# Kernel tuning notes

Measured on AMD Instinct MI355X. Metric: run time of the kernel, lower is better.

The kernel has to match this reference:

```python
import jax, jax.numpy as jnp
import numpy as np

N_NODES = 50000
N_EDGES = 800000
D = 256
N_GRAPHS = 128
N_CLASSES = 2


def gcn_conv(x, W, b, src, dst, ew):
    # PyG GCNConv: add self-loops (weight 1), symmetric norm D^-1/2 (A+I) D^-1/2, then X@W + b
    n = x.shape[0]
    deg = jax.ops.segment_sum(ew, dst, num_segments=n) + 1.0  # includes self-loop weight
    dinv = jnp.where(deg > 0, jax.lax.rsqrt(deg), 0.0)
    xw = x @ W  # [N, D_out]
    norm = dinv[src] * ew * dinv[dst]  # [E]
    msgs = xw[src] * norm[:, None]  # [E, D_out] gathered messages
    agg = jax.ops.segment_sum(msgs, dst, num_segments=n)
    agg = agg + xw * (dinv * dinv)[:, None]  # self-loop contribution
    return agg + b


def setup_inputs() -> dict:
    key = jax.random.key(0)
    ks = jax.random.split(key, 16)
    emb_x = jax.random.normal(ks[0], (N_NODES, D), dtype=jnp.float32)
    edge_index = jax.random.randint(ks[1], (2, N_EDGES), 0, N_NODES, dtype=jnp.int64)
    edge_weight = jax.random.uniform(ks[2], (N_EDGES,), dtype=jnp.float32)
    batch = jnp.sort(jax.random.randint(ks[3], (N_NODES,), 0, N_GRAPHS, dtype=jnp.int64))
    s = 1.0 / np.sqrt(D)
    params = {}
    for i, k in enumerate(ks[4:7]):
        params[f"W{i+1}"] = jax.random.normal(k, (D, D), dtype=jnp.float32) * s
        params[f"b{i+1}"] = jnp.zeros((D,), dtype=jnp.float32)
    params["fc1_w"] = jax.random.normal(ks[7], (2 * D, D), dtype=jnp.float32) / np.sqrt(2 * D)
    params["fc1_b"] = jnp.zeros((D,), dtype=jnp.float32)
    params["fc2_w"] = jax.random.normal(ks[8], (D, N_CLASSES), dtype=jnp.float32) * s
    params["fc2_b"] = jnp.zeros((N_CLASSES,), dtype=jnp.float32)
    return dict(emb_x=emb_x, edge_index=edge_index, edge_weight=edge_weight, batch=batch, **params)


def reference(emb_x, edge_index, edge_weight, batch, W1, b1, W2, b2, W3, b3, fc1_w, fc1_b, fc2_w, fc2_b):
    src, dst = edge_index[0], edge_index[1]
    x = emb_x
    for W, b in ((W1, b1), (W2, b2), (W3, b3)):
        x = gcn_conv(x, W, b, src, dst, edge_weight)
        x = jax.nn.relu(x)  # dropout is identity in eval mode
    counts = jax.ops.segment_sum(jnp.ones((x.shape[0],), x.dtype), batch, num_segments=N_GRAPHS)
    mean_x = jax.ops.segment_sum(x, batch, num_segments=N_GRAPHS) / jnp.maximum(counts, 1.0)[:, None]
    max_x = jax.ops.segment_max(x, batch, num_segments=N_GRAPHS)
    max_x = jnp.where(jnp.isfinite(max_x), max_x, 0.0)  # empty segments -> 0
    h = jnp.concatenate([mean_x, max_x], axis=1)  # [G, 2D]
    h = jax.nn.relu(h @ fc1_w + fc1_b)
    return h @ fc2_w + fc2_b  # [G, n_classes]
```

## Files before the change

kernel.cpp:

```cpp
#include <hip/hip_runtime.h>
#include <math.h>

#define N_NODES 50000
#define N_PAD 50048
#define N_EDGES 800000
#define DIM 256
#define N_GRAPHS 128

using f32x4 = __attribute__((ext_vector_type(4))) float;
using s16x8 = __attribute__((ext_vector_type(8))) short;

__device__ __forceinline__ ushort bf16_hi(float f) {
  unsigned u = __float_as_uint(f);
  return (ushort)((u + 0x7FFFu + ((u >> 16) & 1u)) >> 16);
}
__device__ __forceinline__ float bf16_up(ushort h) {
  return __uint_as_float(((unsigned)h) << 16);
}
__device__ __forceinline__ void bf16_split(float f, ushort& hh, ushort& ll) {
  hh = bf16_hi(f);
  float d = f - bf16_up(hh);
  ll = bf16_hi(d);
}
__device__ __forceinline__ float up_lo(unsigned u) {
  return __uint_as_float(u << 16);
}
__device__ __forceinline__ float up_hi(unsigned u) {
  return __uint_as_float(u & 0xffff0000u);
}

__global__ __launch_bounds__(256) void count_kernel(
    const int* __restrict__ dst, int* __restrict__ counts,
    int* __restrict__ p_local) {
  int e = blockIdx.x * 256 + threadIdx.x;
  if (e < N_EDGES) p_local[e] = atomicAdd(&counts[dst[e]], 1);
}

#define SCAN_CHUNK 1024
#define SCAN_BLOCKS ((N_NODES + SCAN_CHUNK - 1) / SCAN_CHUNK)

__global__ __launch_bounds__(256) void scan_phaseA(
    const int* __restrict__ counts, int* __restrict__ blockSums) {
  __shared__ int sdata[256];
  int b = blockIdx.x, t = threadIdx.x;
  int base = b * SCAN_CHUNK + t * 4;
  int s = 0;
#pragma unroll
  for (int i = 0; i < 4; ++i) {
    int idx = base + i;
    if (idx < N_NODES) s += counts[idx];
  }
  sdata[t] = s;
  __syncthreads();
  for (int off = 128; off > 0; off >>= 1) {
    if (t < off) sdata[t] += sdata[t + off];
    __syncthreads();
  }
  if (t == 0) blockSums[b] = sdata[0];
}

__global__ void scan_phaseB(int* __restrict__ blockSums, int* __restrict__ rs) {
  if (threadIdx.x == 0 && blockIdx.x == 0) {
    int acc = 0;
    for (int i = 0; i < SCAN_BLOCKS; ++i) {
      int v = blockSums[i];
      blockSums[i] = acc;
      acc += v;
    }
    rs[N_NODES] = acc;
  }
}

__global__ __launch_bounds__(256) void scan_phaseC(
    const int* __restrict__ counts, const int* __restrict__ blockSums,
    int* __restrict__ rs) {
  __shared__ int sdata[256];
  int b = blockIdx.x, t = threadIdx.x;
  int base = b * SCAN_CHUNK + t * 4;
  int v[4];
  int s = 0;
#pragma unroll
  for (int i = 0; i < 4; ++i) {
    int idx = base + i;
    v[i] = (idx < N_NODES) ? counts[idx] : 0;
    s += v[i];
  }
  sdata[t] = s;
  __syncthreads();
  for (int off = 1; off < 256; off <<= 1) {
    int x = (t >= off) ? sdata[t - off] : 0;
    __syncthreads();
    sdata[t] += x;
    __syncthreads();
  }
  int excl = (t == 0) ? 0 : sdata[t - 1];
  int o = blockSums[b] + excl;
#pragma unroll
  for (int i = 0; i < 4; ++i) {
    int idx = base + i;
    if (idx < N_NODES) rs[idx] = o;
    o += v[i];
  }
}

__global__ __launch_bounds__(256) void fill_kernel(
    const int* __restrict__ src, const int* __restrict__ dst,
    const float* __restrict__ ew, const int* __restrict__ rs,
    const int* __restrict__ p_local,
    int* __restrict__ csrc, float* __restrict__ cw) {
  int e = blockIdx.x * 256 + threadIdx.x;
  if (e < N_EDGES) {
    int d = dst[e];
    int pos = rs[d] + p_local[e];
    csrc[pos] = src[e];
    cw[pos] = ew[e];
  }
}

__global__ __launch_bounds__(256) void degsum_kernel(
    const int* __restrict__ rs, const float* __restrict__ cw,
    float* __restrict__ dinv) {
  int n = blockIdx.x * 256 + threadIdx.x;
  if (n >= N_NODES) return;
  int b = rs[n], e = rs[n + 1];
  float s = 1.0f;
  for (int i = b; i < e; ++i) s += cw[i];
  dinv[n] = 1.0f / sqrtf(s);
}

__global__ __launch_bounds__(256) void norm_kernel(
    const int* __restrict__ csrc, const float* __restrict__ dinv,
    float* __restrict__ cw) {
  int e = blockIdx.x * 256 + threadIdx.x;
  if (e < N_EDGES) cw[e] = cw[e] * dinv[csrc[e]];
}

__global__ __launch_bounds__(256) void round_x_kernel(
    const float* __restrict__ x, ushort* __restrict__ tab, int n4) {
  int i = blockIdx.x * 256 + threadIdx.x;
  if (i >= n4) return;
  float4 v = ((const float4*)x)[i];
  ushort4 h;
  h.x = bf16_hi(v.x);
  h.y = bf16_hi(v.y);
  h.z = bf16_hi(v.z);
  h.w = bf16_hi(v.w);
  ((ushort4*)tab)[i] = h;
}

__global__ __launch_bounds__(256) void prep_w_kernel(
    const float* __restrict__ W1, const float* __restrict__ W2, const float* __restrict__ W3,
    ushort* __restrict__ wt) {
  int k = blockIdx.x;
  int w = blockIdx.y;
  int n = threadIdx.x;
  const float* W = (w == 0) ? W1 : (w == 1) ? W2 : W3;
  float v = W[k * 256 + n];
  ushort h, l;
  bf16_split(v, h, l);
  ushort* hplane = wt + (size_t)w * 2 * 256 * 256;
  ushort* lplane = hplane + 256 * 256;
  hplane[n * 256 + k] = h;
  lplane[n * 256 + k] = l;
}

#define GBM 64
#define GBK 32

__device__ __forceinline__ void gload16(const void* g, void* l) {
  __builtin_amdgcn_global_load_lds(
      (const __attribute__((address_space(1))) void*)g,
      (__attribute__((address_space(3))) void*)l, 16, 0, 0);
}

__global__ __launch_bounds__(256) void gemm_mfma(
    const ushort* __restrict__ A,
    const ushort* __restrict__ Wh, const ushort* __restrict__ Wl,
    ushort* __restrict__ C, int M) {
  __shared__ ushort Asl[2][GBM * GBK];
  int tid = threadIdx.x;
  int bm = blockIdx.x * GBM;
  int wave = tid >> 6, lane = tid & 63;
  int wc = wave * 64;
  int l15 = lane & 15;
  int lkb = lane >> 4;

  f32x4 acc[4][4];
#pragma unroll
  for (int i = 0; i < 4; ++i)
#pragma unroll
    for (int j = 0; j < 4; ++j) acc[i][j] = (f32x4){0.f, 0.f, 0.f, 0.f};

  int arow = tid & 63, akb = tid >> 6;

#define STAGE_A(buf, ts)                                                       \
  gload16(A + (size_t)(bm + arow) * 256 + (ts) * 32 + akb * 8,                 \
          &Asl[buf][tid * 8])

  STAGE_A(0, 0);
  __syncthreads();
  int cur = 0;
  for (int t = 0; t < 8; ++t) {
    if (t < 7) STAGE_A(cur ^ 1, t + 1);
    s16x8 af[4], bh[4], bl[4];
#pragma unroll
    for (int f = 0; f < 4; ++f) {
      size_t woff = (size_t)(wc + f * 16 + l15) * 256 + t * 32 + lkb * 8;
      bh[f] = *(const s16x8*)(Wh + woff);
      bl[f] = *(const s16x8*)(Wl + woff);
    }
#pragma unroll
    for (int f = 0; f < 4; ++f)
      af[f] = *(const s16x8*)(&Asl[cur][(lkb * 64 + f * 16 + l15) * 8]);
#pragma unroll
    for (int i = 0; i < 4; ++i)
#pragma unroll
      for (int j = 0; j < 4; ++j) {
        acc[i][j] = __builtin_amdgcn_mfma_f32_16x16x32_bf16(af[i], bh[j], acc[i][j], 0, 0, 0);
        acc[i][j] = __builtin_amdgcn_mfma_f32_16x16x32_bf16(af[i], bl[j], acc[i][j], 0, 0, 0);
      }
    __syncthreads();
    cur ^= 1;
  }
#undef STAGE_A

#pragma unroll
  for (int i = 0; i < 4; ++i) {
    int rbase = bm + i * 16 + (lane >> 4) * 4;
#pragma unroll
    for (int j = 0; j < 4; ++j) {
      int col = wc + j * 16 + l15;
#pragma unroll
      for (int r = 0; r < 4; ++r) {
        int row = rbase + r;
        if (row < M) C[(size_t)row * 256 + col] = bf16_hi(acc[i][j][r]);
      }
    }
  }
}

template <int MODE>
__global__ __launch_bounds__(256) void spmm_row(
    const ushort* __restrict__ xw, const int* __restrict__ rs,
    const int* __restrict__ csrc, const float* __restrict__ cw,
    const float* __restrict__ dinv, const float* __restrict__ bias,
    float* __restrict__ xf32, ushort* __restrict__ xout) {
  int wave = threadIdx.x >> 6, lane = threadIdx.x & 63;
  int n = __builtin_amdgcn_readfirstlane(blockIdx.x * 4 + wave);
  const uint2* base = (const uint2*)xw;
  size_t rowoff = (size_t)n * 64 + lane;
  float a0 = 0.f, a1 = 0.f, a2 = 0.f, a3 = 0.f;
  int beg = __builtin_amdgcn_readfirstlane(rs[n]);
  int end = __builtin_amdgcn_readfirstlane(rs[n + 1]);
  int i = beg;
  for (; i + 8 <= end; i += 8) {
    int idx[8];
    float w[8];
    uint2 v[8];
#pragma unroll
    for (int u = 0; u < 8; ++u) { idx[u] = csrc[i + u]; w[u] = cw[i + u]; }
#pragma unroll
    for (int u = 0; u < 8; ++u) v[u] = base[(size_t)idx[u] * 64 + lane];
#pragma unroll
    for (int u = 0; u < 8; ++u) {
      a0 += w[u] * up_lo(v[u].x);
      a1 += w[u] * up_hi(v[u].x);
      a2 += w[u] * up_lo(v[u].y);
      a3 += w[u] * up_hi(v[u].y);
    }
  }
  for (; i < end; ++i) {
    float w0 = cw[i];
    uint2 v0 = base[(size_t)csrc[i] * 64 + lane];
    a0 += w0 * up_lo(v0.x);
    a1 += w0 * up_hi(v0.x);
    a2 += w0 * up_lo(v0.y);
    a3 += w0 * up_hi(v0.y);
  }
  float di = dinv[n];
  float dd = di * di;
  uint2 sv = base[rowoff];
  float4 b = ((const float4*)bias)[lane];
  float r0 = fmaxf(di * a0 + dd * up_lo(sv.x) + b.x, 0.f);
  float r1 = fmaxf(di * a1 + dd * up_hi(sv.x) + b.y, 0.f);
  float r2 = fmaxf(di * a2 + dd * up_lo(sv.y) + b.z, 0.f);
  float r3 = fmaxf(di * a3 + dd * up_hi(sv.y) + b.w, 0.f);
  if (MODE == 1) {
    float4 r;
    r.x = r0; r.y = r1; r.z = r2; r.w = r3;
    ((float4*)xf32)[rowoff] = r;
  } else {
    uint2 hv;
    hv.x = (unsigned)bf16_hi(r0) | ((unsigned)bf16_hi(r1) << 16);
    hv.y = (unsigned)bf16_hi(r2) | ((unsigned)bf16_hi(r3) << 16);
    ((uint2*)xout)[rowoff] = hv;
  }
}

__device__ __forceinline__ int lower_bound_dev(const int* a, int n, int key) {
  int lo = 0, hi = n;
  while (lo < hi) {
    int mid = (lo + hi) >> 1;
    if (a[mid] < key) lo = mid + 1; else hi = mid;
  }
  return lo;
}

__global__ __launch_bounds__(256) void pool_kernel(
    const float* __restrict__ x, const int* __restrict__ batch,
    float* __restrict__ h) {
  int g = blockIdx.x;
  int dchunk = blockIdx.y;
  int t = threadIdx.x;
  int dl = t & 63;
  int nl = t >> 6;
  int d = dchunk * 64 + dl;
  int start = lower_bound_dev(batch, N_NODES, g);
  int end = lower_bound_dev(batch, N_NODES, g + 1);
  float sum = 0.f, mx = 0.f;
  for (int i = start + nl; i < end; i += 4) {
    float v = x[(size_t)i * DIM + d];
    sum += v;
    mx = fmaxf(mx, v);
  }
  __shared__ float ssum[4][64];
  __shared__ float smax[4][64];
  ssum[nl][dl] = sum;
  smax[nl][dl] = mx;
  __syncthreads();
  if (nl == 0) {
    sum = ssum[0][dl] + ssum[1][dl] + ssum[2][dl] + ssum[3][dl];
    mx = fmaxf(fmaxf(smax[0][dl], smax[1][dl]), fmaxf(smax[2][dl], smax[3][dl]));
    float cnt = (float)(end - start);
    h[(size_t)g * (2 * DIM) + d] = sum / fmaxf(cnt, 1.0f);
    h[(size_t)g * (2 * DIM) + DIM + d] = mx;
  }
}

__global__ __launch_bounds__(256) void fc_kernel(
    const float* __restrict__ h, const float* __restrict__ fc1_w,
    const float* __restrict__ fc1_b, const float* __restrict__ fc2_w,
    const float* __restrict__ fc2_b, float* __restrict__ out) {
  int g = blockIdx.x;
  int j = threadIdx.x;
  __shared__ float hs[2 * DIM];
  __shared__ float s0[256], s1[256];
  hs[j] = h[(size_t)g * (2 * DIM) + j];
  hs[j + 256] = h[(size_t)g * (2 * DIM) + 256 + j];
  __syncthreads();
  float acc = fc1_b[j];
  for (int k = 0; k < 2 * DIM; ++k) acc += hs[k] * fc1_w[(size_t)k * DIM + j];
  float r = fmaxf(acc, 0.0f);
  s0[j] = r * fc2_w[j * 2 + 0];
  s1[j] = r * fc2_w[j * 2 + 1];
  __syncthreads();
  for (int off = 128; off > 0; off >>= 1) {
    if (j < off) { s0[j] += s0[j + off]; s1[j] += s1[j + off]; }
    __syncthreads();
  }
  if (j == 0) {
    out[g * 2 + 0] = s0[0] + fc2_b[0];
    out[g * 2 + 1] = s1[0] + fc2_b[1];
  }
}

extern "C" void kernel_launch(void* const* d_in, const int* in_sizes, int n_in,
                              void* d_out, int out_size, void* d_ws, size_t ws_size,
                              hipStream_t stream) {
  const float* emb_x = (const float*)d_in[0];
  const int* eidx = (const int*)d_in[1];
  const int* esrc = eidx;
  const int* edst = eidx + N_EDGES;
  const float* ew = (const float*)d_in[2];
  const int* batch = (const int*)d_in[3];
  const float* W1 = (const float*)d_in[4];
  const float* b1 = (const float*)d_in[5];
  const float* W2 = (const float*)d_in[6];
  const float* b2 = (const float*)d_in[7];
  const float* W3 = (const float*)d_in[8];
  const float* b3 = (const float*)d_in[9];
  const float* fc1_w = (const float*)d_in[10];
  const float* fc1_b = (const float*)d_in[11];
  const float* fc2_w = (const float*)d_in[12];
  const float* fc2_b = (const float*)d_in[13];
  float* out = (float*)d_out;

  char* ws = (char*)d_ws;
  size_t off = 0;
  auto take = [&](size_t bytes) -> char* {
    char* p = ws + off;
    off = (off + bytes + 255) & ~(size_t)255;
    return p;
  };
  ushort* XW = (ushort*)take((size_t)N_PAD * DIM * 2);
  ushort* Xa = (ushort*)take((size_t)N_PAD * DIM * 2);
  float* Xf32 = (float*)take((size_t)N_NODES * DIM * 4);
  ushort* WT = (ushort*)take((size_t)6 * 256 * 256 * 2);
  float* dinv = (float*)take(N_NODES * 4);
  int* counts = (int*)take(N_NODES * 4);
  int* rs = (int*)take((N_NODES + 1) * 4);
  int* p_local = (int*)take(N_EDGES * 4);
  int* blockSums = (int*)take(64 * 4);
  int* csrc = (int*)take(N_EDGES * 4);
  float* cw = (float*)take(N_EDGES * 4);
  float* h = (float*)take((size_t)N_GRAPHS * 2 * DIM * 4);

  hipMemsetAsync(counts, 0, N_NODES * 4, stream);
  hipMemsetAsync(Xa + (size_t)N_NODES * DIM, 0, (size_t)(N_PAD - N_NODES) * DIM * 2, stream);

  int eblocks = (N_EDGES + 255) / 256;
  int nblocks = (N_NODES + 255) / 256;

  count_kernel<<<eblocks, 256, 0, stream>>>(edst, counts, p_local);
  scan_phaseA<<<SCAN_BLOCKS, 256, 0, stream>>>(counts, blockSums);
  scan_phaseB<<<1, 64, 0, stream>>>(blockSums, rs);
  scan_phaseC<<<SCAN_BLOCKS, 256, 0, stream>>>(counts, blockSums, rs);
  fill_kernel<<<eblocks, 256, 0, stream>>>(esrc, edst, ew, rs, p_local, csrc, cw);
  degsum_kernel<<<nblocks, 256, 0, stream>>>(rs, cw, dinv);
  norm_kernel<<<eblocks, 256, 0, stream>>>(csrc, dinv, cw);

  round_x_kernel<<<(N_NODES * DIM / 4 + 255) / 256, 256, 0, stream>>>(
      emb_x, Xa, N_NODES * DIM / 4);
  prep_w_kernel<<<dim3(256, 3), 256, 0, stream>>>(W1, W2, W3, WT);

  ushort* W1h = WT + 0 * 65536; ushort* W1l = WT + 1 * 65536;
  ushort* W2h = WT + 2 * 65536; ushort* W2l = WT + 3 * 65536;
  ushort* W3h = WT + 4 * 65536; ushort* W3l = WT + 5 * 65536;

  dim3 ggrid(N_PAD / GBM);
  int sgrid = N_NODES / 4;

  gemm_mfma<<<ggrid, 256, 0, stream>>>(Xa, W1h, W1l, XW, N_NODES);
  spmm_row<0><<<sgrid, 256, 0, stream>>>(XW, rs, csrc, cw, dinv, b1, nullptr, Xa);
  gemm_mfma<<<ggrid, 256, 0, stream>>>(Xa, W2h, W2l, XW, N_NODES);
  spmm_row<0><<<sgrid, 256, 0, stream>>>(XW, rs, csrc, cw, dinv, b2, nullptr, Xa);
  gemm_mfma<<<ggrid, 256, 0, stream>>>(Xa, W3h, W3l, XW, N_NODES);
  spmm_row<1><<<sgrid, 256, 0, stream>>>(XW, rs, csrc, cw, dinv, b3, Xf32, nullptr);

  pool_kernel<<<dim3(N_GRAPHS, 4), 256, 0, stream>>>(Xf32, batch, h);
  fc_kernel<<<N_GRAPHS, 256, 0, stream>>>(h, fc1_w, fc1_b, fc2_w, fc2_b, out);
}
```

Measured before the change: 460.9 us.

## Prefetch GEMM weight fragments and use 16-byte gathers in SpMM

Result: no change. 452.1 us (-1.9%).

```diff
diff --git a/kernel.cpp b/kernel.cpp
--- a/kernel.cpp
+++ b/kernel.cpp
@@ -21,12 +21,6 @@
   hh = bf16_hi(f);
   float d = f - bf16_up(hh);
   ll = bf16_hi(d);
-}
-__device__ __forceinline__ float up_lo(unsigned u) {
-  return __uint_as_float(u << 16);
-}
-__device__ __forceinline__ float up_hi(unsigned u) {
-  return __uint_as_float(u & 0xffff0000u);
 }
 
 __global__ __launch_bounds__(256) void count_kernel(
@@ -198,29 +192,39 @@
           &Asl[buf][tid * 8])
 
   STAGE_A(0, 0);
-  __syncthreads();
-  int cur = 0;
+  s16x8 bh_c[4], bl_c[4], bh_n[4], bl_n[4];
+#pragma unroll
+  for (int f = 0; f < 4; ++f) {
+    size_t woff = (size_t)(wc + f * 16 + l15) * 256 + lkb * 8;
+    bh_c[f] = *(const s16x8*)(Wh + woff);
+    bl_c[f] = *(const s16x8*)(Wl + woff);
+  }
+  __syncthreads();
+#pragma unroll
   for (int t = 0; t < 8; ++t) {
-    if (t < 7) STAGE_A(cur ^ 1, t + 1);
-    s16x8 af[4], bh[4], bl[4];
-#pragma unroll
-    for (int f = 0; f < 4; ++f) {
-      size_t woff = (size_t)(wc + f * 16 + l15) * 256 + t * 32 + lkb * 8;
-      bh[f] = *(const s16x8*)(Wh + woff);
-      bl[f] = *(const s16x8*)(Wl + woff);
+    if (t < 7) {
+      STAGE_A((t & 1) ^ 1, t + 1);
+#pragma unroll
+      for (int f = 0; f < 4; ++f) {
+        size_t woff = (size_t)(wc + f * 16 + l15) * 256 + (t + 1) * 32 + lkb * 8;
+        bh_n[f] = *(const s16x8*)(Wh + woff);
+        bl_n[f] = *(const s16x8*)(Wl + woff);
+      }
     }
+    s16x8 af[4];
 #pragma unroll
     for (int f = 0; f < 4; ++f)
-      af[f] = *(const s16x8*)(&Asl[cur][(lkb * 64 + f * 16 + l15) * 8]);
+      af[f] = *(const s16x8*)(&Asl[t & 1][(lkb * 64 + f * 16 + l15) * 8]);
 #pragma unroll
     for (int i = 0; i < 4; ++i)
 #pragma unroll
       for (int j = 0; j < 4; ++j) {
-        acc[i][j] = __builtin_amdgcn_mfma_f32_16x16x32_bf16(af[i], bh[j], acc[i][j], 0, 0, 0);
-        acc[i][j] = __builtin_amdgcn_mfma_f32_16x16x32_bf16(af[i], bl[j], acc[i][j], 0, 0, 0);
+        acc[i][j] = __builtin_amdgcn_mfma_f32_16x16x32_bf16(af[i], bh_c[j], acc[i][j], 0, 0, 0);
+        acc[i][j] = __builtin_amdgcn_mfma_f32_16x16x32_bf16(af[i], bl_c[j], acc[i][j], 0, 0, 0);
       }
     __syncthreads();
-    cur ^= 1;
+#pragma unroll
+    for (int f = 0; f < 4; ++f) { bh_c[f] = bh_n[f]; bl_c[f] = bl_n[f]; }
   }
 #undef STAGE_A
 
@@ -240,60 +244,77 @@
 }
 
 template <int MODE>
-__global__ __launch_bounds__(256) void spmm_row(
+__global__ __launch_bounds__(256) void spmm_row16(
     const ushort* __restrict__ xw, const int* __restrict__ rs,
     const int* __restrict__ csrc, const float* __restrict__ cw,
     const float* __restrict__ dinv, const float* __restrict__ bias,
     float* __restrict__ xf32, ushort* __restrict__ xout) {
   int wave = threadIdx.x >> 6, lane = threadIdx.x & 63;
   int n = __builtin_amdgcn_readfirstlane(blockIdx.x * 4 + wave);
-  const uint2* base = (const uint2*)xw;
-  size_t rowoff = (size_t)n * 64 + lane;
-  float a0 = 0.f, a1 = 0.f, a2 = 0.f, a3 = 0.f;
+  int e2 = lane >> 5;
+  int c = lane & 31;
+  const ushort* chunk = xw + c * 8;
+  float acc[8] = {};
   int beg = __builtin_amdgcn_readfirstlane(rs[n]);
   int end = __builtin_amdgcn_readfirstlane(rs[n + 1]);
   int i = beg;
   for (; i + 8 <= end; i += 8) {
-    int idx[8];
-    float w[8];
-    uint2 v[8];
-#pragma unroll
-    for (int u = 0; u < 8; ++u) { idx[u] = csrc[i + u]; w[u] = cw[i + u]; }
-#pragma unroll
-    for (int u = 0; u < 8; ++u) v[u] = base[(size_t)idx[u] * 64 + lane];
-#pragma unroll
-    for (int u = 0; u < 8; ++u) {
-      a0 += w[u] * up_lo(v[u].x);
-      a1 += w[u] * up_hi(v[u].x);
-      a2 += w[u] * up_lo(v[u].y);
-      a3 += w[u] * up_hi(v[u].y);
+    int idx[4];
+    float w[4];
+    s16x8 v[4];
+#pragma unroll
+    for (int u = 0; u < 4; ++u) {
+      idx[u] = csrc[i + 2 * u + e2];
+      w[u] = cw[i + 2 * u + e2];
     }
-  }
-  for (; i < end; ++i) {
-    float w0 = cw[i];
-    uint2 v0 = base[(size_t)csrc[i] * 64 + lane];
-    a0 += w0 * up_lo(v0.x);
-    a1 += w0 * up_hi(v0.x);
-    a2 += w0 * up_lo(v0.y);
-    a3 += w0 * up_hi(v0.y);
-  }
-  float di = dinv[n];
-  float dd = di * di;
-  uint2 sv = base[rowoff];
-  float4 b = ((const float4*)bias)[lane];
-  float r0 = fmaxf(di * a0 + dd * up_lo(sv.x) + b.x, 0.f);
-  float r1 = fmaxf(di * a1 + dd * up_hi(sv.x) + b.y, 0.f);
-  float r2 = fmaxf(di * a2 + dd * up_lo(sv.y) + b.z, 0.f);
-  float r3 = fmaxf(di * a3 + dd * up_hi(sv.y) + b.w, 0.f);
-  if (MODE == 1) {
-    float4 r;
-    r.x = r0; r.y = r1; r.z = r2; r.w = r3;
-    ((float4*)xf32)[rowoff] = r;
-  } else {
-    uint2 hv;
-    hv.x = (unsigned)bf16_hi(r0) | ((unsigned)bf16_hi(r1) << 16);
-    hv.y = (unsigned)bf16_hi(r2) | ((unsigned)bf16_hi(r3) << 16);
-    ((uint2*)xout)[rowoff] = hv;
+#pragma unroll
+    for (int u = 0; u < 4; ++u) v[u] = *(const s16x8*)(chunk + (size_t)idx[u] * 256);
+#pragma unroll
+    for (int u = 0; u < 4; ++u)
+#pragma unroll
+      for (int j = 0; j < 8; ++j) acc[j] += w[u] * bf16_up((ushort)v[u][j]);
+  }
+  for (; i < end; i += 2) {
+    int ii = i + e2;
+    float w = (ii < end) ? cw[ii] : 0.f;
+    int id = csrc[(ii < end) ? ii : (end - 1)];
+    s16x8 v = *(const s16x8*)(chunk + (size_t)id * 256);
+#pragma unroll
+    for (int j = 0; j < 8; ++j) acc[j] += w * bf16_up((ushort)v[j]);
+  }
+#pragma unroll
+  for (int j = 0; j < 8; ++j) acc[j] += __shfl_xor(acc[j], 32);
+  if (e2 == 0) {
+    float di = dinv[n];
+    float dd = di * di;
+    s16x8 sv = *(const s16x8*)(chunk + (size_t)n * 256);
+    int d0 = c * 8;
+    const float4* bb = (const float4*)(bias + d0);
+    float4 b0 = bb[0], b1 = bb[1];
+    float r[8];
+#pragma unroll
+    for (int j = 0; j < 8; ++j) r[j] = di * acc[j] + dd * bf16_up((ushort)sv[j]);
+    r[0] = fmaxf(r[0] + b0.x, 0.f);
+    r[1] = fmaxf(r[1] + b0.y, 0.f);
+    r[2] = fmaxf(r[2] + b0.z, 0.f);
+    r[3] = fmaxf(r[3] + b0.w, 0.f);
+    r[4] = fmaxf(r[4] + b1.x, 0.f);
+    r[5] = fmaxf(r[5] + b1.y, 0.f);
+    r[6] = fmaxf(r[6] + b1.z, 0.f);
+    r[7] = fmaxf(r[7] + b1.w, 0.f);
+    if (MODE == 1) {
+      float4 a0, a1;
+      a0.x = r[0]; a0.y = r[1]; a0.z = r[2]; a0.w = r[3];
+      a1.x = r[4]; a1.y = r[5]; a1.z = r[6]; a1.w = r[7];
+      float* p = xf32 + (size_t)n * 256 + d0;
+      *(float4*)p = a0;
+      *(float4*)(p + 4) = a1;
+    } else {
+      s16x8 hv;
+#pragma unroll
+      for (int j = 0; j < 8; ++j) hv[j] = (short)bf16_hi(r[j]);
+      *(s16x8*)(xout + (size_t)n * 256 + d0) = hv;
+    }
   }
 }
 
@@ -431,11 +452,11 @@
   int sgrid = N_NODES / 4;
 
   gemm_mfma<<<ggrid, 256, 0, stream>>>(Xa, W1h, W1l, XW, N_NODES);
-  spmm_row<0><<<sgrid, 256, 0, stream>>>(XW, rs, csrc, cw, dinv, b1, nullptr, Xa);
+  spmm_row16<0><<<sgrid, 256, 0, stream>>>(XW, rs, csrc, cw, dinv, b1, nullptr, Xa);
   gemm_mfma<<<ggrid, 256, 0, stream>>>(Xa, W2h, W2l, XW, N_NODES);
-  spmm_row<0><<<sgrid, 256, 0, stream>>>(XW, rs, csrc, cw, dinv, b2, nullptr, Xa);
+  spmm_row16<0><<<sgrid, 256, 0, stream>>>(XW, rs, csrc, cw, dinv, b2, nullptr, Xa);
   gemm_mfma<<<ggrid, 256, 0, stream>>>(Xa, W3h, W3l, XW, N_NODES);
-  spmm_row<1><<<sgrid, 256, 0, stream>>>(XW, rs, csrc, cw, dinv, b3, Xf32, nullptr);
+  spmm_row16<1><<<sgrid, 256, 0, stream>>>(XW, rs, csrc, cw, dinv, b3, Xf32, nullptr);
 
   pool_kernel<<<dim3(N_GRAPHS, 4), 256, 0, stream>>>(Xf32, batch, h);
   fc_kernel<<<N_GRAPHS, 256, 0, stream>>>(h, fc1_w, fc1_b, fc2_w, fc2_b, out);
```
